# Kernel optimization log

Hardware: AMD Instinct MI355X
Metric: run time of the kernel (lower is better)

Reference implementation:

```python
import jax, jax.numpy as jnp
import numpy as np

F_CONST = 1.0
B_CONST = 0.1
R_CONST = 0.01
N, DIM = 8192, 64


def setup_inputs() -> dict:
    key = jax.random.key(0)
    k1, k2 = jax.random.split(key)
    x = jax.random.uniform(k1, (N, DIM), dtype=jnp.float32)
    A = jax.random.uniform(k2, (N, N), dtype=jnp.float32)
    return {"t": 0, "x": x, "A": A}


def reference(t, x, A):
    # dx_i/dt = f - b*x_i - diag(A @ (r * x x^T))
    # diag(A @ (x x^T))[i] = sum_j A_ij <x_j, x_i> = <x_i, (A x)_i>
    Ax = A @ x                                      # [N, DIM]
    outer = R_CONST * jnp.sum(x * Ax, axis=1, keepdims=True)  # [N, 1]
    return F_CONST - B_CONST * x - outer            # broadcasts to [N, DIM]
```

## Files before the change

### kernel.cpp

```cpp
#include <hip/hip_runtime.h>

#define N 8192
#define DIM 64
#define KS 256
#define NSUB 32
#define NBUF 4

typedef float f32x4 __attribute__((ext_vector_type(4)));
typedef short bf16x8 __attribute__((ext_vector_type(8)));
typedef unsigned short u16;

__device__ __forceinline__ u16 f32_to_bf16_rne(float f) {
  unsigned int u = __float_as_uint(f);
  return (u16)((u + 0x7FFFu + ((u >> 16) & 1u)) >> 16);
}

__global__ void cvtT_kernel(const float* __restrict__ x, u16* __restrict__ xbT) {
  int t = threadIdx.x;
  int i0 = blockIdx.x * 64;
  int d = t & 63;
  int r = t >> 6;
  int ib = i0 + r * 16;
  alignas(16) u16 v[16];
#pragma unroll
  for (int m = 0; m < 16; ++m)
    v[m] = f32_to_bf16_rne(x[(size_t)(ib + m) * DIM + d]);
  *reinterpret_cast<bf16x8*>(xbT + (size_t)d * N + ib) = *reinterpret_cast<bf16x8*>(&v[0]);
  *reinterpret_cast<bf16x8*>(xbT + (size_t)d * N + ib + 8) = *reinterpret_cast<bf16x8*>(&v[8]);
}

__global__ __launch_bounds__(256, 2) void ax_kernel(const float* __restrict__ A,
                                                    const u16* __restrict__ xbT,
                                                    float* __restrict__ Ax) {
  __shared__ float At[NBUF][16][KS];
  int i0 = blockIdx.x * 16;
  int tid = threadIdx.x;
  int w = tid >> 6, lane = tid & 63;
  int c = lane & 15, q = lane >> 4;

  f32x4 acc[4];
#pragma unroll
  for (int nt = 0; nt < 4; ++nt) acc[nt] = (f32x4){0.f, 0.f, 0.f, 0.f};

#define STAGE(s_)                                                                   \
  {                                                                                 \
    int buf_ = (s_) & (NBUF - 1);                                                   \
    _Pragma("unroll") for (int rr = 0; rr < 4; ++rr) {                              \
      int row_ = w * 4 + rr;                                                        \
      const float* gp_ = A + (size_t)(i0 + row_) * N + (s_)*KS + lane * 4;          \
      __builtin_amdgcn_global_load_lds(                                             \
          (const __attribute__((address_space(1))) unsigned int*)gp_,               \
          (__attribute__((address_space(3))) unsigned int*)&At[buf_][row_][0],      \
          16, 0, 0);                                                                \
    }                                                                               \
  }

  STAGE(0); STAGE(1); STAGE(2);

  for (int s = 0; s < NSUB; ++s) {
    if (s < NSUB - 3) {
      STAGE(s + 3);
      asm volatile("s_waitcnt vmcnt(12)" ::: "memory");
    } else if (s == NSUB - 3) {
      asm volatile("s_waitcnt vmcnt(8)" ::: "memory");
    } else if (s == NSUB - 2) {
      asm volatile("s_waitcnt vmcnt(4)" ::: "memory");
    } else {
      asm volatile("s_waitcnt vmcnt(0)" ::: "memory");
    }
    __builtin_amdgcn_sched_barrier(0);
    __builtin_amdgcn_s_barrier();
    __builtin_amdgcn_sched_barrier(0);

    int buf = s & (NBUF - 1);
#pragma unroll
    for (int t2 = 0; t2 < 2; ++t2) {
      int kk = w * 2 + t2;
      const float* ap = &At[buf][c][kk * 32 + q * 8];
      f32x4 alo = *reinterpret_cast<const f32x4*>(ap);
      f32x4 ahi = *reinterpret_cast<const f32x4*>(ap + 4);
      bf16x8 afv;
      afv[0] = (short)f32_to_bf16_rne(alo[0]);
      afv[1] = (short)f32_to_bf16_rne(alo[1]);
      afv[2] = (short)f32_to_bf16_rne(alo[2]);
      afv[3] = (short)f32_to_bf16_rne(alo[3]);
      afv[4] = (short)f32_to_bf16_rne(ahi[0]);
      afv[5] = (short)f32_to_bf16_rne(ahi[1]);
      afv[6] = (short)f32_to_bf16_rne(ahi[2]);
      afv[7] = (short)f32_to_bf16_rne(ahi[3]);
      const u16* bp = xbT + (size_t)s * KS + kk * 32 + q * 8;
#pragma unroll
      for (int nt = 0; nt < 4; ++nt) {
        bf16x8 bfv = *reinterpret_cast<const bf16x8*>(bp + (size_t)(nt * 16 + c) * N);
        acc[nt] = __builtin_amdgcn_mfma_f32_16x16x32_bf16(afv, bfv, acc[nt], 0, 0, 0);
      }
    }
    __builtin_amdgcn_s_barrier();
    __builtin_amdgcn_sched_barrier(0);
  }
#undef STAGE

  float* Red = &At[0][0][0];
#pragma unroll
  for (int nt = 0; nt < 4; ++nt)
#pragma unroll
    for (int v = 0; v < 4; ++v)
      Red[(w * 16 + q * 4 + v) * 64 + nt * 16 + c] = acc[nt][v];
  __syncthreads();
  int ii = tid >> 4, dq = tid & 15;
  f32x4 sum = *reinterpret_cast<f32x4*>(&Red[(0 * 16 + ii) * 64 + dq * 4]);
#pragma unroll
  for (int ww = 1; ww < 4; ++ww) {
    f32x4 p = *reinterpret_cast<f32x4*>(&Red[(ww * 16 + ii) * 64 + dq * 4]);
    sum += p;
  }
  *reinterpret_cast<f32x4*>(&Ax[(size_t)(i0 + ii) * 64 + dq * 4]) = sum;
}

__global__ void finish_kernel(const float* __restrict__ x,
                              const float* __restrict__ Ax,
                              float* __restrict__ out) {
  int tid = threadIdx.x;
  int i = blockIdx.x * 16 + (tid >> 4);
  int dq = tid & 15;
  size_t base = (size_t)i * DIM + dq * 4;
  f32x4 xv = *reinterpret_cast<const f32x4*>(x + base);
  f32x4 av = *reinterpret_cast<const f32x4*>(Ax + base);
  float p = xv[0] * av[0] + xv[1] * av[1] + xv[2] * av[2] + xv[3] * av[3];
  p += __shfl_xor(p, 1);
  p += __shfl_xor(p, 2);
  p += __shfl_xor(p, 4);
  p += __shfl_xor(p, 8);
  f32x4 o;
  o[0] = 1.0f - 0.1f * xv[0] - 0.01f * p;
  o[1] = 1.0f - 0.1f * xv[1] - 0.01f * p;
  o[2] = 1.0f - 0.1f * xv[2] - 0.01f * p;
  o[3] = 1.0f - 0.1f * xv[3] - 0.01f * p;
  *reinterpret_cast<f32x4*>(out + base) = o;
}

extern "C" void kernel_launch(void* const* d_in, const int* in_sizes, int n_in,
                              void* d_out, int out_size, void* d_ws, size_t ws_size,
                              hipStream_t stream) {
  const float* x = (const float*)d_in[1];
  const float* A = (const float*)d_in[2];
  float* out = (float*)d_out;

  u16* xbT = (u16*)d_ws;
  float* Ax = (float*)((char*)d_ws + (size_t)2 * 1024 * 1024);

  cvtT_kernel<<<128, 256, 0, stream>>>(x, xbT);
  ax_kernel<<<512, 256, 0, stream>>>(A, xbT, Ax);
  finish_kernel<<<512, 256, 0, stream>>>(x, Ax, out);
}
```

Measured before the change: 90.60 us.

## Split-K ax_kernel into 4 K-slices with per-wave private LDS rings

The A@x kernel is split along K into four slices, so 2048 blocks run instead of 512, with occupancy hints raised to 8 blocks per CU. Each wave now streams its own 16x32 tile through a private double-buffered LDS ring, which removes the per-step block-wide barriers. The finish kernel sums the four partial results. The x transpose kernel is rewritten to stage through LDS for coalesced loads. The cost is a 4x larger partial-sum buffer to write and read back, and a shallower prefetch depth per wave.

```diff
diff --git a/kernel.cpp b/kernel.cpp
--- a/kernel.cpp
+++ b/kernel.cpp
@@ -2,9 +2,6 @@
 
 #define N 8192
 #define DIM 64
-#define KS 256
-#define NSUB 32
-#define NBUF 4
 
 typedef float f32x4 __attribute__((ext_vector_type(4)));
 typedef short bf16x8 __attribute__((ext_vector_type(8)));
@@ -16,116 +13,117 @@
 }
 
 __global__ void cvtT_kernel(const float* __restrict__ x, u16* __restrict__ xbT) {
+  __shared__ float st[64][68];
   int t = threadIdx.x;
   int i0 = blockIdx.x * 64;
-  int d = t & 63;
-  int r = t >> 6;
-  int ib = i0 + r * 16;
-  alignas(16) u16 v[16];
+  int r = t >> 2, cq = t & 3;
 #pragma unroll
-  for (int m = 0; m < 16; ++m)
-    v[m] = f32_to_bf16_rne(x[(size_t)(ib + m) * DIM + d]);
-  *reinterpret_cast<bf16x8*>(xbT + (size_t)d * N + ib) = *reinterpret_cast<bf16x8*>(&v[0]);
-  *reinterpret_cast<bf16x8*>(xbT + (size_t)d * N + ib + 8) = *reinterpret_cast<bf16x8*>(&v[8]);
+  for (int m = 0; m < 4; ++m) {
+    f32x4 v = *reinterpret_cast<const f32x4*>(x + (size_t)(i0 + r) * DIM + cq * 16 + m * 4);
+    *reinterpret_cast<f32x4*>(&st[r][cq * 16 + m * 4]) = v;
+  }
+  __syncthreads();
+  int d = t >> 2, iq = t & 3;
+  alignas(16) u16 vb[16];
+#pragma unroll
+  for (int m = 0; m < 16; ++m) vb[m] = f32_to_bf16_rne(st[iq * 16 + m][d]);
+  u16* dst = xbT + (size_t)d * N + i0 + iq * 16;
+  *reinterpret_cast<bf16x8*>(dst) = *reinterpret_cast<bf16x8*>(&vb[0]);
+  *reinterpret_cast<bf16x8*>(dst + 8) = *reinterpret_cast<bf16x8*>(&vb[8]);
 }
 
-__global__ __launch_bounds__(256, 2) void ax_kernel(const float* __restrict__ A,
+__global__ __launch_bounds__(256, 8) void ax_kernel(const float* __restrict__ A,
                                                     const u16* __restrict__ xbT,
-                                                    float* __restrict__ Ax) {
-  __shared__ float At[NBUF][16][KS];
-  int i0 = blockIdx.x * 16;
+                                                    float* __restrict__ spart) {
+  __shared__ float ring[4][2][16][32];
+  int bid = blockIdx.x;
+  int i0 = (bid >> 2) * 16;
+  int kb = bid & 3;
   int tid = threadIdx.x;
   int w = tid >> 6, lane = tid & 63;
   int c = lane & 15, q = lane >> 4;
+  int kwbase = kb * 2048 + w * 512;
+
+  const float* Abase = A + (size_t)(i0 + (lane >> 3)) * N + kwbase + (lane & 7) * 4;
+  const u16* Bbase = xbT + (size_t)c * N + kwbase + q * 8;
 
   f32x4 acc[4];
 #pragma unroll
   for (int nt = 0; nt < 4; ++nt) acc[nt] = (f32x4){0.f, 0.f, 0.f, 0.f};
 
-#define STAGE(s_)                                                                   \
-  {                                                                                 \
-    int buf_ = (s_) & (NBUF - 1);                                                   \
-    _Pragma("unroll") for (int rr = 0; rr < 4; ++rr) {                              \
-      int row_ = w * 4 + rr;                                                        \
-      const float* gp_ = A + (size_t)(i0 + row_) * N + (s_)*KS + lane * 4;          \
-      __builtin_amdgcn_global_load_lds(                                             \
-          (const __attribute__((address_space(1))) unsigned int*)gp_,               \
-          (__attribute__((address_space(3))) unsigned int*)&At[buf_][row_][0],      \
-          16, 0, 0);                                                                \
-    }                                                                               \
+#define STAGE(s_)                                                               \
+  {                                                                             \
+    _Pragma("unroll") for (int e = 0; e < 2; ++e) {                             \
+      const float* gp_ = Abase + (size_t)(e * 8) * N + (s_)*32;                 \
+      __builtin_amdgcn_global_load_lds(                                         \
+          (const __attribute__((address_space(1))) unsigned int*)gp_,           \
+          (__attribute__((address_space(3))) unsigned int*)&ring[w][(s_)&1][e * 8][0], \
+          16, 0, 0);                                                            \
+    }                                                                           \
   }
 
-  STAGE(0); STAGE(1); STAGE(2);
+  STAGE(0);
 
-  for (int s = 0; s < NSUB; ++s) {
-    if (s < NSUB - 3) {
-      STAGE(s + 3);
-      asm volatile("s_waitcnt vmcnt(12)" ::: "memory");
-    } else if (s == NSUB - 3) {
-      asm volatile("s_waitcnt vmcnt(8)" ::: "memory");
-    } else if (s == NSUB - 2) {
-      asm volatile("s_waitcnt vmcnt(4)" ::: "memory");
+#pragma unroll
+  for (int s = 0; s < 16; ++s) {
+    if (s < 15) {
+      STAGE(s + 1);
+      asm volatile("s_waitcnt vmcnt(2)" ::: "memory");
     } else {
       asm volatile("s_waitcnt vmcnt(0)" ::: "memory");
     }
     __builtin_amdgcn_sched_barrier(0);
-    __builtin_amdgcn_s_barrier();
-    __builtin_amdgcn_sched_barrier(0);
 
-    int buf = s & (NBUF - 1);
+    const float* ap = &ring[w][s & 1][c][q * 8];
+    f32x4 lo = *reinterpret_cast<const f32x4*>(ap);
+    f32x4 hi = *reinterpret_cast<const f32x4*>(ap + 4);
+    bf16x8 afv;
+    afv[0] = (short)f32_to_bf16_rne(lo[0]);
+    afv[1] = (short)f32_to_bf16_rne(lo[1]);
+    afv[2] = (short)f32_to_bf16_rne(lo[2]);
+    afv[3] = (short)f32_to_bf16_rne(lo[3]);
+    afv[4] = (short)f32_to_bf16_rne(hi[0]);
+    afv[5] = (short)f32_to_bf16_rne(hi[1]);
+    afv[6] = (short)f32_to_bf16_rne(hi[2]);
+    afv[7] = (short)f32_to_bf16_rne(hi[3]);
+
+    const u16* bp = Bbase + s * 32;
 #pragma unroll
-    for (int t2 = 0; t2 < 2; ++t2) {
-      int kk = w * 2 + t2;
-      const float* ap = &At[buf][c][kk * 32 + q * 8];
-      f32x4 alo = *reinterpret_cast<const f32x4*>(ap);
-      f32x4 ahi = *reinterpret_cast<const f32x4*>(ap + 4);
-      bf16x8 afv;
-      afv[0] = (short)f32_to_bf16_rne(alo[0]);
-      afv[1] = (short)f32_to_bf16_rne(alo[1]);
-      afv[2] = (short)f32_to_bf16_rne(alo[2]);
-      afv[3] = (short)f32_to_bf16_rne(alo[3]);
-      afv[4] = (short)f32_to_bf16_rne(ahi[0]);
-      afv[5] = (short)f32_to_bf16_rne(ahi[1]);
-      afv[6] = (short)f32_to_bf16_rne(ahi[2]);
-      afv[7] = (short)f32_to_bf16_rne(ahi[3]);
-      const u16* bp = xbT + (size_t)s * KS + kk * 32 + q * 8;
-#pragma unroll
-      for (int nt = 0; nt < 4; ++nt) {
-        bf16x8 bfv = *reinterpret_cast<const bf16x8*>(bp + (size_t)(nt * 16 + c) * N);
-        acc[nt] = __builtin_amdgcn_mfma_f32_16x16x32_bf16(afv, bfv, acc[nt], 0, 0, 0);
-      }
+    for (int nt = 0; nt < 4; ++nt) {
+      bf16x8 bfv = *reinterpret_cast<const bf16x8*>(bp + (size_t)(nt * 16) * N);
+      acc[nt] = __builtin_amdgcn_mfma_f32_16x16x32_bf16(afv, bfv, acc[nt], 0, 0, 0);
     }
-    __builtin_amdgcn_s_barrier();
-    __builtin_amdgcn_sched_barrier(0);
   }
 #undef STAGE
 
-  float* Red = &At[0][0][0];
+  __syncthreads();
+  float* red = (float*)ring;
 #pragma unroll
   for (int nt = 0; nt < 4; ++nt)
 #pragma unroll
     for (int v = 0; v < 4; ++v)
-      Red[(w * 16 + q * 4 + v) * 64 + nt * 16 + c] = acc[nt][v];
+      red[(w * 16 + q * 4 + v) * 64 + nt * 16 + c] = acc[nt][v];
   __syncthreads();
   int ii = tid >> 4, dq = tid & 15;
-  f32x4 sum = *reinterpret_cast<f32x4*>(&Red[(0 * 16 + ii) * 64 + dq * 4]);
+  f32x4 sum = *reinterpret_cast<f32x4*>(&red[(0 * 16 + ii) * 64 + dq * 4]);
 #pragma unroll
-  for (int ww = 1; ww < 4; ++ww) {
-    f32x4 p = *reinterpret_cast<f32x4*>(&Red[(ww * 16 + ii) * 64 + dq * 4]);
-    sum += p;
-  }
-  *reinterpret_cast<f32x4*>(&Ax[(size_t)(i0 + ii) * 64 + dq * 4]) = sum;
+  for (int ww = 1; ww < 4; ++ww)
+    sum += *reinterpret_cast<f32x4*>(&red[(ww * 16 + ii) * 64 + dq * 4]);
+  *reinterpret_cast<f32x4*>(&spart[((size_t)kb * N + i0 + ii) * 64 + dq * 4]) = sum;
 }
 
 __global__ void finish_kernel(const float* __restrict__ x,
-                              const float* __restrict__ Ax,
+                              const float* __restrict__ spart,
                               float* __restrict__ out) {
   int tid = threadIdx.x;
   int i = blockIdx.x * 16 + (tid >> 4);
   int dq = tid & 15;
   size_t base = (size_t)i * DIM + dq * 4;
   f32x4 xv = *reinterpret_cast<const f32x4*>(x + base);
-  f32x4 av = *reinterpret_cast<const f32x4*>(Ax + base);
+  f32x4 av = *reinterpret_cast<const f32x4*>(spart + base);
+#pragma unroll
+  for (int kb = 1; kb < 4; ++kb)
+    av += *reinterpret_cast<const f32x4*>(spart + (size_t)kb * N * DIM + base);
   float p = xv[0] * av[0] + xv[1] * av[1] + xv[2] * av[2] + xv[3] * av[3];
   p += __shfl_xor(p, 1);
   p += __shfl_xor(p, 2);
@@ -147,9 +145,9 @@
   float* out = (float*)d_out;
 
   u16* xbT = (u16*)d_ws;
-  float* Ax = (float*)((char*)d_ws + (size_t)2 * 1024 * 1024);
+  float* spart = (float*)((char*)d_ws + (size_t)2 * 1024 * 1024);
 
   cvtT_kernel<<<128, 256, 0, stream>>>(x, xbT);
-  ax_kernel<<<512, 256, 0, stream>>>(A, xbT, Ax);
-  finish_kernel<<<512, 256, 0, stream>>>(x, Ax, out);
+  ax_kernel<<<2048, 256, 0, stream>>>(A, xbT, spart);
+  finish_kernel<<<512, 256, 0, stream>>>(x, spart, out);
 }
```

Measured after the change: 99.33 us. 1.1x slower.
